# Kernel optimization log

Measured on AMD Instinct MI355X. Metric: run time of the kernel, lower is better.

Reference implementation:

```python
import jax, jax.numpy as jnp
import numpy as np

N_NODES = 100000
SAMPLES = 16


def setup_inputs() -> dict:
    key = jax.random.key(0)
    ks = jax.random.split(key, 9)
    x = jax.random.normal(ks[0], (N_NODES, 128), dtype=jnp.float32)
    neigh_idx = jax.random.randint(ks[1], (N_NODES, SAMPLES), 0, N_NODES)
    batch = jax.random.randint(ks[2], (8192,), 0, N_NODES)
    W1 = jax.random.normal(ks[3], (256, 128), dtype=jnp.float32) * 0.05
    b1 = jax.random.normal(ks[4], (128,), dtype=jnp.float32) * 0.05
    W2 = jax.random.normal(ks[5], (256, 128), dtype=jnp.float32) * 0.05
    b2 = jax.random.normal(ks[6], (128,), dtype=jnp.float32) * 0.05
    Wout = jax.random.normal(ks[7], (128, 64), dtype=jnp.float32) * 0.05
    bout = jax.random.normal(ks[8], (64,), dtype=jnp.float32) * 0.05
    return {"x": x, "neigh_idx": neigh_idx, "batch": batch,
            "W1": W1, "b1": b1, "W2": W2, "b2": b2,
            "Wout": Wout, "bout": bout}


def _sage_layer(h, neigh_idx, W, b):
    # h: [N, d]; gather sampled neighbors -> [N, S, d]; max-aggregate; concat-linear
    neigh = h[neigh_idx]                     # irregular gather, memory-bound core
    agg = jnp.max(neigh, axis=1)             # MaxAggregation over samples
    feats = jnp.concatenate([h, agg], axis=-1)  # [N, 2d]
    return feats @ W + b


def reference(x, neigh_idx, batch, W1, b1, W2, b2, Wout, bout):
    # layer 1: relu(Linear(concat(x, max_neigh(x))))
    h1 = jax.nn.relu(_sage_layer(x, neigh_idx, W1, b1))
    # layer 2 (== n_layers): Linear output (no relu) fed straight into proj_out
    h2 = _sage_layer(h1, neigh_idx, W2, b2)
    out = h2 @ Wout + bout                   # proj_out (Dropout is eval identity)
    return out[batch]
```

## Files before the change

kernel.cpp:

```cpp
#include <hip/hip_runtime.h>
#include <cmath>
#include <cstdint>

#define N_NODES 100000
#define SAMPLES 16
#define DIM 128
#define NBATCH 8192

#define FSTR 264
#define H2STR 132

typedef _Float16 half8 __attribute__((ext_vector_type(8)));
typedef float floatx4 __attribute__((ext_vector_type(4)));

__device__ __forceinline__ half8 h8max(half8 a, half8 b) {
    half8 r;
#pragma unroll
    for (int i = 0; i < 8; ++i) r[i] = (a[i] > b[i]) ? a[i] : b[i];
    return r;
}

__global__ __launch_bounds__(256) void setup_kernel(
    const float* __restrict__ x,
    const float* __restrict__ W1,
    const float* __restrict__ W2,
    const int* __restrict__ batch,
    const int* __restrict__ nidx,
    int* __restrict__ flags,
    _Float16* __restrict__ xh,
    _Float16* __restrict__ W1sw,
    _Float16* __restrict__ W2sw) {
    const int bid = blockIdx.x;
    if (bid < 6250) {
        const size_t base = ((size_t)bid * 256 + threadIdx.x) * 8;
        const float4* xp = (const float4*)(x + base);
        const float4 a = xp[0], b = xp[1];
        half8 v;
        v[0] = (_Float16)a.x; v[1] = (_Float16)a.y;
        v[2] = (_Float16)a.z; v[3] = (_Float16)a.w;
        v[4] = (_Float16)b.x; v[5] = (_Float16)b.y;
        v[6] = (_Float16)b.z; v[7] = (_Float16)b.w;
        *(half8*)(xh + base) = v;
    } else if (bid < 6282) {
        const int tid = (bid - 6250) * 256 + threadIdx.x;
        const int which = tid >> 12;
        const int r = tid & 4095;
        const int kb = r >> 9, nb = (r >> 6) & 7, lane = r & 63;
        const int q = lane >> 4, c = lane & 15;
        const float* W = which ? W2 : W1;
        _Float16* O = which ? W2sw : W1sw;
        const int k0 = kb * 32 + q * 8;
        const int n = nb * 16 + c;
        half8 v;
#pragma unroll
        for (int j = 0; j < 8; ++j) v[j] = (_Float16)W[(size_t)(k0 + j) * DIM + n];
        *(half8*)(O + (size_t)r * 8) = v;
    } else {
        const int j = (bid - 6282) * 256 + threadIdx.x;
        if (j < NBATCH) {
            const int b = batch[j];
            flags[b] = 1;
            const int* row = nidx + (size_t)b * SAMPLES;
#pragma unroll
            for (int s = 0; s < SAMPLES; ++s) flags[row[s]] = 1;
        }
    }
}

__global__ __launch_bounds__(256) void layer1_kernel(
    const _Float16* __restrict__ xh,
    const int* __restrict__ nidx,
    const _Float16* __restrict__ W1sw,
    const float* __restrict__ b1,
    const int* __restrict__ flags,
    _Float16* __restrict__ h1h) {
    const int t = threadIdx.x;
    const int g = t >> 4;
    const int cl = t & 15;
    const int i0 = blockIdx.x * 16;
    const int i = i0 + g;

    __shared__ __align__(16) _Float16 feats[16 * FSTR];

    const bool fi = (flags[i] == 1);
    if (fi) {
        const char* xb = (const char*)xh;
        const int cb = cl * 16;
        const half8 self = *(const half8*)(xb + (size_t)i * 256 + cb);
        const int4* ip = (const int4*)(nidx + (size_t)i * SAMPLES);
        const int4 a0 = ip[0], a1 = ip[1], a2 = ip[2], a3 = ip[3];
        int off[16];
        off[0]  = a0.x * 256 + cb; off[1]  = a0.y * 256 + cb;
        off[2]  = a0.z * 256 + cb; off[3]  = a0.w * 256 + cb;
        off[4]  = a1.x * 256 + cb; off[5]  = a1.y * 256 + cb;
        off[6]  = a1.z * 256 + cb; off[7]  = a1.w * 256 + cb;
        off[8]  = a2.x * 256 + cb; off[9]  = a2.y * 256 + cb;
        off[10] = a2.z * 256 + cb; off[11] = a2.w * 256 + cb;
        off[12] = a3.x * 256 + cb; off[13] = a3.y * 256 + cb;
        off[14] = a3.z * 256 + cb; off[15] = a3.w * 256 + cb;
        half8 v[16];
#pragma unroll
        for (int s = 0; s < 16; ++s) v[s] = *(const half8*)(xb + off[s]);
#pragma unroll
        for (int s = 0; s < 8; ++s) v[s] = h8max(v[s], v[s + 8]);
#pragma unroll
        for (int s = 0; s < 4; ++s) v[s] = h8max(v[s], v[s + 4]);
        const half8 mx = h8max(h8max(v[0], v[1]), h8max(v[2], v[3]));
        *(half8*)(feats + g * FSTR + cl * 8) = self;
        *(half8*)(feats + g * FSTR + DIM + cl * 8) = mx;
    } else {
        half8 z;
#pragma unroll
        for (int e = 0; e < 8; ++e) z[e] = (_Float16)0.f;
        *(half8*)(feats + g * FSTR + cl * 8) = z;
        *(half8*)(feats + g * FSTR + DIM + cl * 8) = z;
    }
    __syncthreads();

    const int wave = t >> 6;
    const int lane = t & 63;
    const int q = lane >> 4, c = lane & 15;
    const int nb0 = wave * 2;
    floatx4 acc[2];
    acc[0] = (floatx4){0.f, 0.f, 0.f, 0.f};
    acc[1] = (floatx4){0.f, 0.f, 0.f, 0.f};
#pragma unroll
    for (int kb = 0; kb < 8; ++kb) {
        const half8 a = *(const half8*)(feats + c * FSTR + kb * 32 + q * 8);
#pragma unroll
        for (int j = 0; j < 2; ++j) {
            const half8 b = *(const half8*)(W1sw + (size_t)((kb * 8 + nb0 + j) * 64 + lane) * 8);
            acc[j] = __builtin_amdgcn_mfma_f32_16x16x32_f16(a, b, acc[j], 0, 0, 0);
        }
    }

#pragma unroll
    for (int r = 0; r < 4; ++r) {
        const int node = i0 + q * 4 + r;
        if (flags[node] != 1) continue;
#pragma unroll
        for (int j = 0; j < 2; ++j) {
            const int n = (nb0 + j) * 16 + c;
            const float v = fmaxf(acc[j][r] + b1[n], 0.f);
            h1h[(size_t)node * DIM + n] = (_Float16)v;
        }
    }
}

__global__ __launch_bounds__(256) void layer2_kernel(
    const _Float16* __restrict__ h1h,
    const int* __restrict__ nidx,
    const int* __restrict__ batch,
    const _Float16* __restrict__ W2sw,
    const float* __restrict__ b2,
    const float* __restrict__ Wout,
    const float* __restrict__ bout,
    float* __restrict__ out) {
    const int t = threadIdx.x;
    const int wave = t >> 6;
    const int lane = t & 63;
    const int q = lane >> 4, c = lane & 15;
    const int w0 = blockIdx.x * 16;

    __shared__ __align__(16) _Float16 feats[16 * FSTR];
    __shared__ __align__(16) float h2s[16 * H2STR];

    {
        const int m = t >> 4;
        const int cl = t & 15;
        const int node = batch[w0 + m];
        const char* hb = (const char*)h1h;
        const int cb = cl * 16;
        const half8 self = *(const half8*)(hb + (size_t)node * 256 + cb);
        const int4* ip = (const int4*)(nidx + (size_t)node * SAMPLES);
        const int4 a0 = ip[0], a1 = ip[1], a2 = ip[2], a3 = ip[3];
        int off[16];
        off[0]  = a0.x * 256 + cb; off[1]  = a0.y * 256 + cb;
        off[2]  = a0.z * 256 + cb; off[3]  = a0.w * 256 + cb;
        off[4]  = a1.x * 256 + cb; off[5]  = a1.y * 256 + cb;
        off[6]  = a1.z * 256 + cb; off[7]  = a1.w * 256 + cb;
        off[8]  = a2.x * 256 + cb; off[9]  = a2.y * 256 + cb;
        off[10] = a2.z * 256 + cb; off[11] = a2.w * 256 + cb;
        off[12] = a3.x * 256 + cb; off[13] = a3.y * 256 + cb;
        off[14] = a3.z * 256 + cb; off[15] = a3.w * 256 + cb;
        half8 v[16];
#pragma unroll
        for (int s = 0; s < 16; ++s) v[s] = *(const half8*)(hb + off[s]);
#pragma unroll
        for (int s = 0; s < 8; ++s) v[s] = h8max(v[s], v[s + 8]);
#pragma unroll
        for (int s = 0; s < 4; ++s) v[s] = h8max(v[s], v[s + 4]);
        const half8 mx = h8max(h8max(v[0], v[1]), h8max(v[2], v[3]));
        *(half8*)(feats + m * FSTR + cl * 8) = self;
        *(half8*)(feats + m * FSTR + DIM + cl * 8) = mx;
    }
    __syncthreads();

    const int nb0 = wave * 2;
    floatx4 acc[2];
    acc[0] = (floatx4){0.f, 0.f, 0.f, 0.f};
    acc[1] = (floatx4){0.f, 0.f, 0.f, 0.f};
#pragma unroll
    for (int kb = 0; kb < 8; ++kb) {
        const half8 a = *(const half8*)(feats + c * FSTR + kb * 32 + q * 8);
#pragma unroll
        for (int j = 0; j < 2; ++j) {
            const half8 b = *(const half8*)(W2sw + (size_t)((kb * 8 + nb0 + j) * 64 + lane) * 8);
            acc[j] = __builtin_amdgcn_mfma_f32_16x16x32_f16(a, b, acc[j], 0, 0, 0);
        }
    }
#pragma unroll
    for (int j = 0; j < 2; ++j) {
        const int n = (nb0 + j) * 16 + c;
        const float bias = b2[n];
#pragma unroll
        for (int r = 0; r < 4; ++r)
            h2s[(q * 4 + r) * H2STR + n] = acc[j][r] + bias;
    }
    __syncthreads();

    float accs[4];
    const float bo = bout[lane];
#pragma unroll
    for (int r = 0; r < 4; ++r) accs[r] = bo;
    for (int k4 = 0; k4 < DIM; k4 += 4) {
        float wv[4];
#pragma unroll
        for (int j = 0; j < 4; ++j) wv[j] = Wout[(size_t)(k4 + j) * 64 + lane];
#pragma unroll
        for (int r = 0; r < 4; ++r) {
            const float4 f = *(const float4*)&h2s[(wave * 4 + r) * H2STR + k4];
            accs[r] += f.x * wv[0] + f.y * wv[1] + f.z * wv[2] + f.w * wv[3];
        }
    }
#pragma unroll
    for (int r = 0; r < 4; ++r)
        out[(size_t)(w0 + wave * 4 + r) * 64 + lane] = accs[r];
}

extern "C" void kernel_launch(void* const* d_in, const int* in_sizes, int n_in,
                              void* d_out, int out_size, void* d_ws, size_t ws_size,
                              hipStream_t stream) {
    const float* x    = (const float*)d_in[0];
    const int* nidx   = (const int*)d_in[1];
    const int* batch  = (const int*)d_in[2];
    const float* W1   = (const float*)d_in[3];
    const float* b1   = (const float*)d_in[4];
    const float* W2   = (const float*)d_in[5];
    const float* b2   = (const float*)d_in[6];
    const float* Wout = (const float*)d_in[7];
    const float* bout = (const float*)d_in[8];
    float* out        = (float*)d_out;

    int* flags      = (int*)d_ws;
    _Float16* W1sw  = (_Float16*)((char*)d_ws + 409600);
    _Float16* W2sw  = (_Float16*)((char*)d_ws + 475136);
    _Float16* xh    = (_Float16*)((char*)d_ws + 540672);
    _Float16* h1h   = (_Float16*)((char*)d_ws + 26140672);

    setup_kernel<<<6314, 256, 0, stream>>>(x, W1, W2, batch, nidx, flags, xh, W1sw, W2sw);
    layer1_kernel<<<N_NODES / 16, 256, 0, stream>>>(xh, nidx, W1sw, b1, flags, h1h);
    layer2_kernel<<<NBATCH / 16, 256, 0, stream>>>(h1h, nidx, batch, W2sw, b2, Wout, bout, out);
}
```

Baseline: 173.4 us.

## Split layer-1 into separate neighbor-gather kernel and register-fed MFMA GEMM kernel

The fused layer-1 kernel is split in two. A gather kernel computes the max over sampled neighbors and writes it to the h1 buffer. A new GEMM kernel then loads the self and aggregated rows straight into registers, and each wave computes all 128 output columns for 16 nodes, with no shared-memory staging or block barrier. The aim is to decouple the latency-bound gather from the MFMA work and to drop the shared-memory round-trip. The cost is an extra kernel launch and an extra global write and read of the aggregated features. The GEMM also reads and writes the same buffer in place, which is only safe because each wave owns its own rows.

```diff
diff --git a/kernel.cpp b/kernel.cpp
--- a/kernel.cpp
+++ b/kernel.cpp
@@ -67,81 +67,93 @@
     }
 }
 
-__global__ __launch_bounds__(256) void layer1_kernel(
+__global__ __launch_bounds__(256) void gather_kernel(
     const _Float16* __restrict__ xh,
     const int* __restrict__ nidx,
+    const int* __restrict__ flags,
+    _Float16* __restrict__ aggh) {
+    const int t = threadIdx.x;
+    const int g = t >> 4;
+    const int cl = t & 15;
+    const int i = blockIdx.x * 16 + g;
+    if (flags[i] != 1) return;
+
+    const char* xb = (const char*)xh;
+    const int cb = cl * 16;
+    const int4* ip = (const int4*)(nidx + (size_t)i * SAMPLES);
+    const int4 a0 = ip[0], a1 = ip[1], a2 = ip[2], a3 = ip[3];
+    int off[16];
+    off[0]  = a0.x * 256 + cb; off[1]  = a0.y * 256 + cb;
+    off[2]  = a0.z * 256 + cb; off[3]  = a0.w * 256 + cb;
+    off[4]  = a1.x * 256 + cb; off[5]  = a1.y * 256 + cb;
+    off[6]  = a1.z * 256 + cb; off[7]  = a1.w * 256 + cb;
+    off[8]  = a2.x * 256 + cb; off[9]  = a2.y * 256 + cb;
+    off[10] = a2.z * 256 + cb; off[11] = a2.w * 256 + cb;
+    off[12] = a3.x * 256 + cb; off[13] = a3.y * 256 + cb;
+    off[14] = a3.z * 256 + cb; off[15] = a3.w * 256 + cb;
+    half8 v[16];
+#pragma unroll
+    for (int s = 0; s < 16; ++s) v[s] = *(const half8*)(xb + off[s]);
+#pragma unroll
+    for (int s = 0; s < 8; ++s) v[s] = h8max(v[s], v[s + 8]);
+#pragma unroll
+    for (int s = 0; s < 4; ++s) v[s] = h8max(v[s], v[s + 4]);
+    const half8 mx = h8max(h8max(v[0], v[1]), h8max(v[2], v[3]));
+    *(half8*)((char*)aggh + (size_t)i * 256 + cb) = mx;
+}
+
+__global__ __launch_bounds__(256) void gemm1_kernel(
+    const _Float16* __restrict__ xh,
+    const _Float16* aggh,
     const _Float16* __restrict__ W1sw,
     const float* __restrict__ b1,
     const int* __restrict__ flags,
-    _Float16* __restrict__ h1h) {
+    _Float16* h1h) {
     const int t = threadIdx.x;
-    const int g = t >> 4;
-    const int cl = t & 15;
-    const int i0 = blockIdx.x * 16;
-    const int i = i0 + g;
-
-    __shared__ __align__(16) _Float16 feats[16 * FSTR];
-
-    const bool fi = (flags[i] == 1);
-    if (fi) {
-        const char* xb = (const char*)xh;
-        const int cb = cl * 16;
-        const half8 self = *(const half8*)(xb + (size_t)i * 256 + cb);
-        const int4* ip = (const int4*)(nidx + (size_t)i * SAMPLES);
-        const int4 a0 = ip[0], a1 = ip[1], a2 = ip[2], a3 = ip[3];
-        int off[16];
-        off[0]  = a0.x * 256 + cb; off[1]  = a0.y * 256 + cb;
-        off[2]  = a0.z * 256 + cb; off[3]  = a0.w * 256 + cb;
-        off[4]  = a1.x * 256 + cb; off[5]  = a1.y * 256 + cb;
-        off[6]  = a1.z * 256 + cb; off[7]  = a1.w * 256 + cb;
-        off[8]  = a2.x * 256 + cb; off[9]  = a2.y * 256 + cb;
-        off[10] = a2.z * 256 + cb; off[11] = a2.w * 256 + cb;
-        off[12] = a3.x * 256 + cb; off[13] = a3.y * 256 + cb;
-        off[14] = a3.z * 256 + cb; off[15] = a3.w * 256 + cb;
-        half8 v[16];
-#pragma unroll
-        for (int s = 0; s < 16; ++s) v[s] = *(const half8*)(xb + off[s]);
-#pragma unroll
-        for (int s = 0; s < 8; ++s) v[s] = h8max(v[s], v[s + 8]);
-#pragma unroll
-        for (int s = 0; s < 4; ++s) v[s] = h8max(v[s], v[s + 4]);
-        const half8 mx = h8max(h8max(v[0], v[1]), h8max(v[2], v[3]));
-        *(half8*)(feats + g * FSTR + cl * 8) = self;
-        *(half8*)(feats + g * FSTR + DIM + cl * 8) = mx;
-    } else {
-        half8 z;
-#pragma unroll
-        for (int e = 0; e < 8; ++e) z[e] = (_Float16)0.f;
-        *(half8*)(feats + g * FSTR + cl * 8) = z;
-        *(half8*)(feats + g * FSTR + DIM + cl * 8) = z;
-    }
-    __syncthreads();
-
     const int wave = t >> 6;
     const int lane = t & 63;
     const int q = lane >> 4, c = lane & 15;
-    const int nb0 = wave * 2;
-    floatx4 acc[2];
-    acc[0] = (floatx4){0.f, 0.f, 0.f, 0.f};
-    acc[1] = (floatx4){0.f, 0.f, 0.f, 0.f};
+    const int w0 = blockIdx.x * 64 + wave * 16;
+
+    const int i = w0 + c;
+    const bool fi = (i < N_NODES) && (flags[i] == 1);
+
+    half8 sk[4], mk[4];
+#pragma unroll
+    for (int j = 0; j < 4; ++j)
+#pragma unroll
+        for (int e = 0; e < 8; ++e) { sk[j][e] = (_Float16)0.f; mk[j][e] = (_Float16)0.f; }
+
+    if (fi) {
+        const _Float16* sp = xh + (size_t)i * DIM + q * 8;
+        const _Float16* mp = aggh + (size_t)i * DIM + q * 8;
+#pragma unroll
+        for (int j = 0; j < 4; ++j) sk[j] = *(const half8*)(sp + j * 32);
+#pragma unroll
+        for (int j = 0; j < 4; ++j) mk[j] = *(const half8*)(mp + j * 32);
+    }
+
+    floatx4 acc[8];
+#pragma unroll
+    for (int nb = 0; nb < 8; ++nb) acc[nb] = (floatx4){0.f, 0.f, 0.f, 0.f};
 #pragma unroll
     for (int kb = 0; kb < 8; ++kb) {
-        const half8 a = *(const half8*)(feats + c * FSTR + kb * 32 + q * 8);
-#pragma unroll
-        for (int j = 0; j < 2; ++j) {
-            const half8 b = *(const half8*)(W1sw + (size_t)((kb * 8 + nb0 + j) * 64 + lane) * 8);
-            acc[j] = __builtin_amdgcn_mfma_f32_16x16x32_f16(a, b, acc[j], 0, 0, 0);
+        const half8 a = (kb < 4) ? sk[kb] : mk[kb - 4];
+#pragma unroll
+        for (int nb = 0; nb < 8; ++nb) {
+            const half8 b = *(const half8*)(W1sw + (size_t)((kb * 8 + nb) * 64 + lane) * 8);
+            acc[nb] = __builtin_amdgcn_mfma_f32_16x16x32_f16(a, b, acc[nb], 0, 0, 0);
         }
     }
 
 #pragma unroll
     for (int r = 0; r < 4; ++r) {
-        const int node = i0 + q * 4 + r;
-        if (flags[node] != 1) continue;
-#pragma unroll
-        for (int j = 0; j < 2; ++j) {
-            const int n = (nb0 + j) * 16 + c;
-            const float v = fmaxf(acc[j][r] + b1[n], 0.f);
+        const int node = w0 + q * 4 + r;
+        if (node >= N_NODES || flags[node] != 1) continue;
+#pragma unroll
+        for (int nb = 0; nb < 8; ++nb) {
+            const int n = nb * 16 + c;
+            const float v = fmaxf(acc[nb][r] + b1[n], 0.f);
             h1h[(size_t)node * DIM + n] = (_Float16)v;
         }
     }
@@ -259,6 +271,7 @@
     _Float16* h1h   = (_Float16*)((char*)d_ws + 26140672);
 
     setup_kernel<<<6314, 256, 0, stream>>>(x, W1, W2, batch, nidx, flags, xh, W1sw, W2sw);
-    layer1_kernel<<<N_NODES / 16, 256, 0, stream>>>(xh, nidx, W1sw, b1, flags, h1h);
+    gather_kernel<<<N_NODES / 16, 256, 0, stream>>>(xh, nidx, flags, h1h);
+    gemm1_kernel<<<(N_NODES + 63) / 64, 256, 0, stream>>>(xh, h1h, W1sw, b1, flags, h1h);
     layer2_kernel<<<NBATCH / 16, 256, 0, stream>>>(h1h, nidx, batch, W2sw, b2, Wout, bout, out);
 }
```

Measured after the change: 186.8 us. +7.7%, slower.

## Process two node tiles per layer-1 block, overlapping second gather with first MFMA

Applied to the files above, without the earlier changes.

Layer 1 now handles 32 nodes per block in two 16-node tiles held in a double-buffered shared array. The neighbour gather for the second tile is issued before the MFMA of the first tile, so memory latency can overlap with matrix work. The grid is halved, and a launch-bounds occupancy hint of 6 blocks per CU is added. This costs double the shared memory per block and possible register pressure from the occupancy hint.

```diff
diff --git a/kernel.cpp b/kernel.cpp
--- a/kernel.cpp
+++ b/kernel.cpp
@@ -67,27 +67,15 @@
     }
 }
 
-__global__ __launch_bounds__(256) void layer1_kernel(
-    const _Float16* __restrict__ xh,
-    const int* __restrict__ nidx,
-    const _Float16* __restrict__ W1sw,
-    const float* __restrict__ b1,
-    const int* __restrict__ flags,
-    _Float16* __restrict__ h1h) {
-    const int t = threadIdx.x;
-    const int g = t >> 4;
-    const int cl = t & 15;
-    const int i0 = blockIdx.x * 16;
-    const int i = i0 + g;
-
-    __shared__ __align__(16) _Float16 feats[16 * FSTR];
-
-    const bool fi = (flags[i] == 1);
-    if (fi) {
-        const char* xb = (const char*)xh;
-        const int cb = cl * 16;
-        const half8 self = *(const half8*)(xb + (size_t)i * 256 + cb);
-        const int4* ip = (const int4*)(nidx + (size_t)i * SAMPLES);
+__device__ __forceinline__ void gather16(
+    const _Float16* __restrict__ xh, const int* __restrict__ nidx,
+    const int* __restrict__ flags, _Float16* buf, int node, int slot, int cl) {
+    const char* xb = (const char*)xh;
+    const int cb = cl * 16;
+    half8 self, mx;
+    if (flags[node] == 1) {
+        self = *(const half8*)(xb + (size_t)node * 256 + cb);
+        const int4* ip = (const int4*)(nidx + (size_t)node * SAMPLES);
         const int4 a0 = ip[0], a1 = ip[1], a2 = ip[2], a3 = ip[3];
         int off[16];
         off[0]  = a0.x * 256 + cb; off[1]  = a0.y * 256 + cb;
@@ -105,20 +93,19 @@
         for (int s = 0; s < 8; ++s) v[s] = h8max(v[s], v[s + 8]);
 #pragma unroll
         for (int s = 0; s < 4; ++s) v[s] = h8max(v[s], v[s + 4]);
-        const half8 mx = h8max(h8max(v[0], v[1]), h8max(v[2], v[3]));
-        *(half8*)(feats + g * FSTR + cl * 8) = self;
-        *(half8*)(feats + g * FSTR + DIM + cl * 8) = mx;
+        mx = h8max(h8max(v[0], v[1]), h8max(v[2], v[3]));
     } else {
-        half8 z;
-#pragma unroll
-        for (int e = 0; e < 8; ++e) z[e] = (_Float16)0.f;
-        *(half8*)(feats + g * FSTR + cl * 8) = z;
-        *(half8*)(feats + g * FSTR + DIM + cl * 8) = z;
-    }
-    __syncthreads();
-
-    const int wave = t >> 6;
-    const int lane = t & 63;
+#pragma unroll
+        for (int e = 0; e < 8; ++e) { self[e] = (_Float16)0.f; mx[e] = (_Float16)0.f; }
+    }
+    *(half8*)(buf + slot * FSTR + cl * 8) = self;
+    *(half8*)(buf + slot * FSTR + DIM + cl * 8) = mx;
+}
+
+__device__ __forceinline__ void mfma16(
+    const _Float16* buf, const _Float16* __restrict__ Wsw,
+    const float* __restrict__ bias, const int* __restrict__ flags,
+    _Float16* __restrict__ h1h, int tbase, int wave, int lane) {
     const int q = lane >> 4, c = lane & 15;
     const int nb0 = wave * 2;
     floatx4 acc[2];
@@ -126,25 +113,50 @@
     acc[1] = (floatx4){0.f, 0.f, 0.f, 0.f};
 #pragma unroll
     for (int kb = 0; kb < 8; ++kb) {
-        const half8 a = *(const half8*)(feats + c * FSTR + kb * 32 + q * 8);
+        const half8 a = *(const half8*)(buf + c * FSTR + kb * 32 + q * 8);
 #pragma unroll
         for (int j = 0; j < 2; ++j) {
-            const half8 b = *(const half8*)(W1sw + (size_t)((kb * 8 + nb0 + j) * 64 + lane) * 8);
+            const half8 b = *(const half8*)(Wsw + (size_t)((kb * 8 + nb0 + j) * 64 + lane) * 8);
             acc[j] = __builtin_amdgcn_mfma_f32_16x16x32_f16(a, b, acc[j], 0, 0, 0);
         }
     }
-
 #pragma unroll
     for (int r = 0; r < 4; ++r) {
-        const int node = i0 + q * 4 + r;
+        const int node = tbase + q * 4 + r;
         if (flags[node] != 1) continue;
 #pragma unroll
         for (int j = 0; j < 2; ++j) {
             const int n = (nb0 + j) * 16 + c;
-            const float v = fmaxf(acc[j][r] + b1[n], 0.f);
+            const float v = fmaxf(acc[j][r] + bias[n], 0.f);
             h1h[(size_t)node * DIM + n] = (_Float16)v;
         }
     }
+}
+
+__global__ __launch_bounds__(256, 6) void layer1_kernel(
+    const _Float16* __restrict__ xh,
+    const int* __restrict__ nidx,
+    const _Float16* __restrict__ W1sw,
+    const float* __restrict__ b1,
+    const int* __restrict__ flags,
+    _Float16* __restrict__ h1h) {
+    const int t = threadIdx.x;
+    const int g = t >> 4;
+    const int cl = t & 15;
+    const int wave = t >> 6;
+    const int lane = t & 63;
+    const int base = blockIdx.x * 32;
+
+    __shared__ __align__(16) _Float16 feats[2][16 * FSTR];
+
+    gather16(xh, nidx, flags, feats[0], base + g, g, cl);
+    __syncthreads();
+
+    gather16(xh, nidx, flags, feats[1], base + 16 + g, g, cl);
+    mfma16(feats[0], W1sw, b1, flags, h1h, base, wave, lane);
+    __syncthreads();
+
+    mfma16(feats[1], W1sw, b1, flags, h1h, base + 16, wave, lane);
 }
 
 __global__ __launch_bounds__(256) void layer2_kernel(
@@ -259,6 +271,6 @@
     _Float16* h1h   = (_Float16*)((char*)d_ws + 26140672);
 
     setup_kernel<<<6314, 256, 0, stream>>>(x, W1, W2, batch, nidx, flags, xh, W1sw, W2sw);
-    layer1_kernel<<<N_NODES / 16, 256, 0, stream>>>(xh, nidx, W1sw, b1, flags, h1h);
+    layer1_kernel<<<N_NODES / 32, 256, 0, stream>>>(xh, nidx, W1sw, b1, flags, h1h);
     layer2_kernel<<<NBATCH / 16, 256, 0, stream>>>(h1h, nidx, batch, W2sw, b2, Wout, bout, out);
 }
```

Result: no change. 173.4 us (-0.0%).

## Software-pipeline layer1 gather with MFMA over two 32-node tiles per block

Applied to the files above, without the earlier changes.

Layer 1 now uses 512-thread blocks that handle 64 nodes as two 32-node halves. The W1 fragments are loaded into registers once per block, and the neighbor gather for the second half is issued before the MFMA on the first half, so gather latency overlaps with matrix work. This costs more registers and 2× shared memory per block, and makes each block larger and coarser. Bounds checks were added for the final partial block.

```diff
diff --git a/kernel.cpp b/kernel.cpp
--- a/kernel.cpp
+++ b/kernel.cpp
@@ -67,7 +67,7 @@
     }
 }
 
-__global__ __launch_bounds__(256) void layer1_kernel(
+__global__ __launch_bounds__(512, 2) void layer1_kernel(
     const _Float16* __restrict__ xh,
     const int* __restrict__ nidx,
     const _Float16* __restrict__ W1sw,
@@ -77,72 +77,148 @@
     const int t = threadIdx.x;
     const int g = t >> 4;
     const int cl = t & 15;
-    const int i0 = blockIdx.x * 16;
-    const int i = i0 + g;
-
-    __shared__ __align__(16) _Float16 feats[16 * FSTR];
-
-    const bool fi = (flags[i] == 1);
-    if (fi) {
-        const char* xb = (const char*)xh;
-        const int cb = cl * 16;
-        const half8 self = *(const half8*)(xb + (size_t)i * 256 + cb);
-        const int4* ip = (const int4*)(nidx + (size_t)i * SAMPLES);
-        const int4 a0 = ip[0], a1 = ip[1], a2 = ip[2], a3 = ip[3];
-        int off[16];
-        off[0]  = a0.x * 256 + cb; off[1]  = a0.y * 256 + cb;
-        off[2]  = a0.z * 256 + cb; off[3]  = a0.w * 256 + cb;
-        off[4]  = a1.x * 256 + cb; off[5]  = a1.y * 256 + cb;
-        off[6]  = a1.z * 256 + cb; off[7]  = a1.w * 256 + cb;
-        off[8]  = a2.x * 256 + cb; off[9]  = a2.y * 256 + cb;
-        off[10] = a2.z * 256 + cb; off[11] = a2.w * 256 + cb;
-        off[12] = a3.x * 256 + cb; off[13] = a3.y * 256 + cb;
-        off[14] = a3.z * 256 + cb; off[15] = a3.w * 256 + cb;
-        half8 v[16];
-#pragma unroll
-        for (int s = 0; s < 16; ++s) v[s] = *(const half8*)(xb + off[s]);
-#pragma unroll
-        for (int s = 0; s < 8; ++s) v[s] = h8max(v[s], v[s + 8]);
-#pragma unroll
-        for (int s = 0; s < 4; ++s) v[s] = h8max(v[s], v[s + 4]);
-        const half8 mx = h8max(h8max(v[0], v[1]), h8max(v[2], v[3]));
-        *(half8*)(feats + g * FSTR + cl * 8) = self;
-        *(half8*)(feats + g * FSTR + DIM + cl * 8) = mx;
-    } else {
-        half8 z;
-#pragma unroll
-        for (int e = 0; e < 8; ++e) z[e] = (_Float16)0.f;
-        *(half8*)(feats + g * FSTR + cl * 8) = z;
-        *(half8*)(feats + g * FSTR + DIM + cl * 8) = z;
-    }
-    __syncthreads();
-
     const int wave = t >> 6;
     const int lane = t & 63;
     const int q = lane >> 4, c = lane & 15;
-    const int nb0 = wave * 2;
-    floatx4 acc[2];
-    acc[0] = (floatx4){0.f, 0.f, 0.f, 0.f};
-    acc[1] = (floatx4){0.f, 0.f, 0.f, 0.f};
-#pragma unroll
-    for (int kb = 0; kb < 8; ++kb) {
-        const half8 a = *(const half8*)(feats + c * FSTR + kb * 32 + q * 8);
-#pragma unroll
-        for (int j = 0; j < 2; ++j) {
-            const half8 b = *(const half8*)(W1sw + (size_t)((kb * 8 + nb0 + j) * 64 + lane) * 8);
-            acc[j] = __builtin_amdgcn_mfma_f32_16x16x32_f16(a, b, acc[j], 0, 0, 0);
-        }
-    }
-
-#pragma unroll
-    for (int r = 0; r < 4; ++r) {
-        const int node = i0 + q * 4 + r;
-        if (flags[node] != 1) continue;
-#pragma unroll
-        for (int j = 0; j < 2; ++j) {
-            const int n = (nb0 + j) * 16 + c;
-            const float v = fmaxf(acc[j][r] + b1[n], 0.f);
-            h1h[(size_t)node * DIM + n] = (_Float16)v;
+    const int base = blockIdx.x * 64;
+
+    __shared__ __align__(16) _Float16 feats[2][32 * FSTR];
+
+    half8 bfr[8];
+#pragma unroll
+    for (int kb = 0; kb < 8; ++kb)
+        bfr[kb] = *(const half8*)(W1sw + (size_t)((kb * 8 + wave) * 64 + lane) * 8);
+
+    {
+        const int i = base + g;
+        const bool fi = (i < N_NODES) && (flags[i] == 1);
+        half8 self, mx;
+        if (fi) {
+            const char* xb = (const char*)xh;
+            const int cb = cl * 16;
+            self = *(const half8*)(xb + (size_t)i * 256 + cb);
+            const int4* ip = (const int4*)(nidx + (size_t)i * SAMPLES);
+            const int4 a0 = ip[0], a1 = ip[1], a2 = ip[2], a3 = ip[3];
+            int off[16];
+            off[0]  = a0.x * 256 + cb; off[1]  = a0.y * 256 + cb;
+            off[2]  = a0.z * 256 + cb; off[3]  = a0.w * 256 + cb;
+            off[4]  = a1.x * 256 + cb; off[5]  = a1.y * 256 + cb;
+            off[6]  = a1.z * 256 + cb; off[7]  = a1.w * 256 + cb;
+            off[8]  = a2.x * 256 + cb; off[9]  = a2.y * 256 + cb;
+            off[10] = a2.z * 256 + cb; off[11] = a2.w * 256 + cb;
+            off[12] = a3.x * 256 + cb; off[13] = a3.y * 256 + cb;
+            off[14] = a3.z * 256 + cb; off[15] = a3.w * 256 + cb;
+            half8 v[16];
+#pragma unroll
+            for (int s = 0; s < 16; ++s) v[s] = *(const half8*)(xb + off[s]);
+#pragma unroll
+            for (int s = 0; s < 8; ++s) v[s] = h8max(v[s], v[s + 8]);
+#pragma unroll
+            for (int s = 0; s < 4; ++s) v[s] = h8max(v[s], v[s + 4]);
+            mx = h8max(h8max(v[0], v[1]), h8max(v[2], v[3]));
+        } else {
+#pragma unroll
+            for (int e = 0; e < 8; ++e) { self[e] = (_Float16)0.f; mx[e] = (_Float16)0.f; }
+        }
+        *(half8*)(feats[0] + g * FSTR + cl * 8) = self;
+        *(half8*)(feats[0] + g * FSTR + DIM + cl * 8) = mx;
+    }
+    __syncthreads();
+
+    const int n1 = base + 32 + g;
+    const bool f1 = (n1 < N_NODES) && (flags[n1] == 1);
+    half8 v1[16], self1;
+    const int cb = cl * 16;
+    if (f1) {
+        const char* xb = (const char*)xh;
+        const int4* ip = (const int4*)(nidx + (size_t)n1 * SAMPLES);
+        const int4 a0 = ip[0], a1 = ip[1], a2 = ip[2], a3 = ip[3];
+        self1 = *(const half8*)(xb + (size_t)n1 * 256 + cb);
+        v1[0]  = *(const half8*)(xb + (size_t)(a0.x * 256 + cb));
+        v1[1]  = *(const half8*)(xb + (size_t)(a0.y * 256 + cb));
+        v1[2]  = *(const half8*)(xb + (size_t)(a0.z * 256 + cb));
+        v1[3]  = *(const half8*)(xb + (size_t)(a0.w * 256 + cb));
+        v1[4]  = *(const half8*)(xb + (size_t)(a1.x * 256 + cb));
+        v1[5]  = *(const half8*)(xb + (size_t)(a1.y * 256 + cb));
+        v1[6]  = *(const half8*)(xb + (size_t)(a1.z * 256 + cb));
+        v1[7]  = *(const half8*)(xb + (size_t)(a1.w * 256 + cb));
+        v1[8]  = *(const half8*)(xb + (size_t)(a2.x * 256 + cb));
+        v1[9]  = *(const half8*)(xb + (size_t)(a2.y * 256 + cb));
+        v1[10] = *(const half8*)(xb + (size_t)(a2.z * 256 + cb));
+        v1[11] = *(const half8*)(xb + (size_t)(a2.w * 256 + cb));
+        v1[12] = *(const half8*)(xb + (size_t)(a3.x * 256 + cb));
+        v1[13] = *(const half8*)(xb + (size_t)(a3.y * 256 + cb));
+        v1[14] = *(const half8*)(xb + (size_t)(a3.z * 256 + cb));
+        v1[15] = *(const half8*)(xb + (size_t)(a3.w * 256 + cb));
+    }
+    __builtin_amdgcn_sched_barrier(0);
+
+    floatx4 acc0[2];
+    acc0[0] = (floatx4){0.f, 0.f, 0.f, 0.f};
+    acc0[1] = (floatx4){0.f, 0.f, 0.f, 0.f};
+#pragma unroll
+    for (int ms = 0; ms < 2; ++ms) {
+        const _Float16* fp = feats[0] + (ms * 16 + c) * FSTR;
+#pragma unroll
+        for (int kb = 0; kb < 8; ++kb) {
+            const half8 a = *(const half8*)(fp + kb * 32 + q * 8);
+            acc0[ms] = __builtin_amdgcn_mfma_f32_16x16x32_f16(a, bfr[kb], acc0[ms], 0, 0, 0);
+        }
+    }
+    __builtin_amdgcn_sched_barrier(0);
+
+    if (f1) {
+#pragma unroll
+        for (int s = 0; s < 8; ++s) v1[s] = h8max(v1[s], v1[s + 8]);
+#pragma unroll
+        for (int s = 0; s < 4; ++s) v1[s] = h8max(v1[s], v1[s + 4]);
+        const half8 mx = h8max(h8max(v1[0], v1[1]), h8max(v1[2], v1[3]));
+        *(half8*)(feats[1] + g * FSTR + cl * 8) = self1;
+        *(half8*)(feats[1] + g * FSTR + DIM + cl * 8) = mx;
+    } else {
+        half8 z;
+#pragma unroll
+        for (int e = 0; e < 8; ++e) z[e] = (_Float16)0.f;
+        *(half8*)(feats[1] + g * FSTR + cl * 8) = z;
+        *(half8*)(feats[1] + g * FSTR + DIM + cl * 8) = z;
+    }
+
+    const int n = wave * 16 + c;
+    const float bias = b1[n];
+#pragma unroll
+    for (int ms = 0; ms < 2; ++ms) {
+#pragma unroll
+        for (int r = 0; r < 4; ++r) {
+            const int node = base + ms * 16 + q * 4 + r;
+            if (node < N_NODES && flags[node] == 1) {
+                const float val = fmaxf(acc0[ms][r] + bias, 0.f);
+                h1h[(size_t)node * DIM + n] = (_Float16)val;
+            }
+        }
+    }
+    __syncthreads();
+
+    floatx4 acc1[2];
+    acc1[0] = (floatx4){0.f, 0.f, 0.f, 0.f};
+    acc1[1] = (floatx4){0.f, 0.f, 0.f, 0.f};
+#pragma unroll
+    for (int ms = 0; ms < 2; ++ms) {
+        const _Float16* fp = feats[1] + (ms * 16 + c) * FSTR;
+#pragma unroll
+        for (int kb = 0; kb < 8; ++kb) {
+            const half8 a = *(const half8*)(fp + kb * 32 + q * 8);
+            acc1[ms] = __builtin_amdgcn_mfma_f32_16x16x32_f16(a, bfr[kb], acc1[ms], 0, 0, 0);
+        }
+    }
+#pragma unroll
+    for (int ms = 0; ms < 2; ++ms) {
+#pragma unroll
+        for (int r = 0; r < 4; ++r) {
+            const int node = base + 32 + ms * 16 + q * 4 + r;
+            if (node < N_NODES && flags[node] == 1) {
+                const float val = fmaxf(acc1[ms][r] + bias, 0.f);
+                h1h[(size_t)node * DIM + n] = (_Float16)val;
+            }
         }
     }
 }
@@ -259,6 +335,6 @@
     _Float16* h1h   = (_Float16*)((char*)d_ws + 26140672);
 
     setup_kernel<<<6314, 256, 0, stream>>>(x, W1, W2, batch, nidx, flags, xh, W1sw, W2sw);
-    layer1_kernel<<<N_NODES / 16, 256, 0, stream>>>(xh, nidx, W1sw, b1, flags, h1h);
+    layer1_kernel<<<(N_NODES + 63) / 64, 512, 0, stream>>>(xh, nidx, W1sw, b1, flags, h1h);
     layer2_kernel<<<NBATCH / 16, 256, 0, stream>>>(h1h, nidx, batch, W2sw, b2, Wout, bout, out);
 }
```

Result: slower. 198.7 us (+14.6%).
